# Kernel tuning notes

Measured on AMD Instinct MI355X. Metric: run time of the kernel, lower is better.

Reference implementation:

```python
import jax, jax.numpy as jnp
import numpy as np

H, DH = 8, 64  # num_heads, head_dim


def setup_inputs() -> dict:
    key = jax.random.key(0)
    ks = jax.random.split(key, 7)
    m, nq, nkv, d = 4, 2048, 2048, 512
    return {
        "xq": jax.random.normal(ks[0], (m, nq, d), jnp.float32),
        "xk": jax.random.normal(ks[1], (m, nkv, d), jnp.float32),
        "xv": jax.random.normal(ks[2], (m, nkv, d), jnp.float32),
        "Wq": jax.random.normal(ks[3], (d, H * DH), jnp.float32) * 0.02,
        "Wk": jax.random.normal(ks[4], (d, H * DH), jnp.float32) * 0.02,
        "Wv": jax.random.normal(ks[5], (d, H * DH), jnp.float32) * 0.02,
        "Wo": jax.random.normal(ks[6], (H * DH, d), jnp.float32) * 0.02,
        "bo": jnp.zeros((d,), jnp.float32),
    }


def _split_heads(t):
    # [b, n, h*d] -> [b, h, n, d]
    b, n, _ = t.shape
    return t.reshape(b, n, H, DH).transpose(0, 2, 1, 3)


def reference(xq, xk, xv, Wq, Wk, Wv, Wo, bo):
    scale = DH ** -0.5
    q = _split_heads(xq @ Wq)   # [b,h,nq,dh]
    k = _split_heads(xk @ Wk)   # [b,h,nkv,dh]
    v = _split_heads(xv @ Wv)   # [b,h,nkv,dh]
    dots = jnp.einsum("bhqd,bhkd->bhqk", q, k) * scale  # [b,h,nq,nkv]
    # diagonal attention term: query attends to its own (k,v) projection
    xq_k = _split_heads(xq @ Wk)
    xq_v = _split_heads(xq @ Wv)
    diag = jnp.sum(q * xq_k, axis=-1, keepdims=True) * scale  # [b,h,nq,1]
    dots = jnp.concatenate([dots, diag], axis=-1)  # [b,h,nq,nkv+1]
    attn = jax.nn.softmax(dots, axis=-1)
    out = jnp.einsum("bhqk,bhkd->bhqd", attn[..., :-1], v) + attn[..., -1:] * xq_v
    b, _, nq, _ = out.shape
    out = out.transpose(0, 2, 1, 3).reshape(b, nq, H * DH)  # merge heads
    return out @ Wo + bo
```

## Files before the change

### kernel.cpp

```cpp
#include <hip/hip_runtime.h>

#define LOG2E 1.44269504088896f
#define CS (0.125f * LOG2E)

typedef __bf16 bf16x8 __attribute__((ext_vector_type(8)));
typedef float f32x4 __attribute__((ext_vector_type(4)));
typedef float f32x16 __attribute__((ext_vector_type(16)));
typedef unsigned short u16x8 __attribute__((ext_vector_type(8)));

#if __has_builtin(__builtin_amdgcn_exp2f)
#define fexp2(x) __builtin_amdgcn_exp2f(x)
#else
extern "C" __device__ float __ocml_native_exp2_f32(float);
#define fexp2(x) __ocml_native_exp2_f32(x)
#endif

__device__ __forceinline__ unsigned short f2bf(float f) {
  union { float f; unsigned int u; } v{f};
  unsigned int r = v.u + 0x7fffu + ((v.u >> 16) & 1u);
  return (unsigned short)(r >> 16);
}
__device__ __forceinline__ float bf2f(unsigned short u) {
  union { unsigned int u; float f; } v; v.u = ((unsigned int)u) << 16; return v.f;
}
__device__ __forceinline__ unsigned int pkr(float a, float b) {
  unsigned int ua = __builtin_bit_cast(unsigned int, a) + 0x8000u;
  unsigned int ub = __builtin_bit_cast(unsigned int, b) + 0x8000u;
  return __builtin_amdgcn_perm(ub, ua, 0x07060302);
}

#define PLSWAP(x, y) asm("v_permlane32_swap_b32 %0, %1" : "+v"(x), "+v"(y))

typedef __attribute__((address_space(3))) unsigned int lds32_t;
typedef const __attribute__((address_space(1))) unsigned int glb32_t;
__device__ __forceinline__ void gld16(const unsigned short* g, unsigned short* l) {
  __builtin_amdgcn_global_load_lds((glb32_t*)(unsigned long long)g,
                                   (lds32_t*)(unsigned int)(unsigned long long)l,
                                   16, 0, 0);
}

__global__ __launch_bounds__(256) void conv_all(
    const float* __restrict__ xq, const float* __restrict__ xk, const float* __restrict__ xv,
    const float* __restrict__ Wq, const float* __restrict__ Wk,
    const float* __restrict__ Wv, const float* __restrict__ Wo,
    unsigned short* __restrict__ oxq, unsigned short* __restrict__ oxk, unsigned short* __restrict__ oxv,
    unsigned short* __restrict__ oWq, unsigned short* __restrict__ oWk,
    unsigned short* __restrict__ oWv, unsigned short* __restrict__ oWo) {
  __shared__ unsigned short T[64 * 65];
  const int blk = blockIdx.x;
  if (blk < 12288) {
    const int N4 = (8192 * 512) / 4;
    int idx = blk * 256 + threadIdx.x;
    const float* src; unsigned short* dst; int i;
    if (idx < N4)          { src = xq; dst = oxq; i = idx; }
    else if (idx < 2 * N4) { src = xk; dst = oxk; i = idx - N4; }
    else                   { src = xv; dst = oxv; i = idx - 2 * N4; }
    float4 v = ((const float4*)src)[i];
    ushort4 o; o.x = f2bf(v.x); o.y = f2bf(v.y); o.z = f2bf(v.z); o.w = f2bf(v.w);
    ((ushort4*)dst)[i] = o;
  } else {
    const int wblk = blk - 12288;
    const int wsel = wblk >> 6;
    const int tile = wblk & 63;
    const int tk = (tile >> 3) * 64, tn = (tile & 7) * 64;
    const float* src = (wsel == 0) ? Wq : (wsel == 1) ? Wk : (wsel == 2) ? Wv : Wo;
    unsigned short* dst = (wsel == 0) ? oWq : (wsel == 1) ? oWk : (wsel == 2) ? oWv : oWo;
    const float scale = (wsel == 0) ? CS : 1.0f;
    const int rr = threadIdx.x >> 4;
    const int cc = (threadIdx.x & 15) * 4;
#pragma unroll
    for (int i = 0; i < 4; i++) {
      int row = rr + i * 16;
      float4 v = *(const float4*)&src[(size_t)(tk + row) * 512 + tn + cc];
      T[(cc + 0) * 65 + row] = f2bf(v.x * scale);
      T[(cc + 1) * 65 + row] = f2bf(v.y * scale);
      T[(cc + 2) * 65 + row] = f2bf(v.z * scale);
      T[(cc + 3) * 65 + row] = f2bf(v.w * scale);
    }
    __syncthreads();
#pragma unroll
    for (int i = 0; i < 4; i++) {
      int n = rr + i * 16;
      ushort4 o;
      o.x = T[n * 65 + cc + 0]; o.y = T[n * 65 + cc + 1];
      o.z = T[n * 65 + cc + 2]; o.w = T[n * 65 + cc + 3];
      *(ushort4*)&dst[(size_t)(tn + n) * 512 + tk + cc] = o;
    }
  }
}

__device__ __forceinline__ void gemm_tile(
    const unsigned short* __restrict__ A, const unsigned short* __restrict__ Bt,
    int rowBlk, int colBlk, unsigned short* As, unsigned short* Bs, f32x4 (&acc)[4][4]) {
  const int t = threadIdx.x;
  const int lane = t & 63, c = lane & 15, g = lane >> 4;
  const int w = t >> 6;
  const int wm = w & 1, wn = w >> 1;
#pragma unroll
  for (int i = 0; i < 4; i++)
#pragma unroll
    for (int j = 0; j < 4; j++)
#pragma unroll
      for (int r = 0; r < 4; r++) acc[i][j][r] = 0.f;

  const int sr = t >> 2, sch = t & 3;
#define STAGE_PROJ(kkk, buf)                                                     \
  do {                                                                           \
    unsigned short* Ad = As + (buf) * (128 * 32);                                \
    unsigned short* Bd = Bs + (buf) * (128 * 32);                                \
    gld16(&A[(size_t)(rowBlk + sr) * 512 + (kkk) + sch * 8], &Ad[t * 8]);        \
    gld16(&Bt[(size_t)(colBlk + sr) * 512 + (kkk) + sch * 8], &Bd[t * 8]);       \
    gld16(&A[(size_t)(rowBlk + sr + 64) * 512 + (kkk) + sch * 8],                \
          &Ad[(t + 256) * 8]);                                                   \
    gld16(&Bt[(size_t)(colBlk + sr + 64) * 512 + (kkk) + sch * 8],               \
          &Bd[(t + 256) * 8]);                                                   \
  } while (0)

  STAGE_PROJ(0, 0);
  __syncthreads();

  for (int kt = 0; kt < 16; kt++) {
    if (kt < 15) STAGE_PROJ((kt + 1) * 32, (kt + 1) & 1);
    const unsigned short* Ac = As + (kt & 1) * (128 * 32);
    const unsigned short* Bc = Bs + (kt & 1) * (128 * 32);
    bf16x8 af[4], bfr[4];
#pragma unroll
    for (int i = 0; i < 4; i++)
      af[i] = __builtin_bit_cast(bf16x8, *(const u16x8*)&Ac[(wm * 64 + i * 16 + c) * 32 + g * 8]);
#pragma unroll
    for (int j = 0; j < 4; j++)
      bfr[j] = __builtin_bit_cast(bf16x8, *(const u16x8*)&Bc[(wn * 64 + j * 16 + c) * 32 + g * 8]);
#pragma unroll
    for (int i = 0; i < 4; i++)
#pragma unroll
      for (int j = 0; j < 4; j++)
        acc[i][j] = __builtin_amdgcn_mfma_f32_16x16x32_bf16(af[i], bfr[j], acc[i][j], 0, 0, 0);
    if (kt < 15) __syncthreads();
  }
#undef STAGE_PROJ
}

__global__ __launch_bounds__(256) void proj_all(
    const unsigned short* __restrict__ xq, const unsigned short* __restrict__ xk,
    const unsigned short* __restrict__ xv,
    const unsigned short* __restrict__ Wq, const unsigned short* __restrict__ Wk,
    const unsigned short* __restrict__ Wv,
    unsigned short* __restrict__ Qo, unsigned short* __restrict__ XKo,
    unsigned short* __restrict__ XVo, unsigned short* __restrict__ Ko,
    unsigned short* __restrict__ Vto) {
  __shared__ unsigned short As[2 * 128 * 32];
  __shared__ unsigned short Bs[2 * 128 * 32];
  const int rowBlk = blockIdx.x * 128;
  const int y = blockIdx.y;
  const unsigned short* A; const unsigned short* Bt; int colBlk; int mode;
  unsigned short* out;
  if (y < 12) {
    int wsel = y >> 2;
    A = xq; colBlk = (y & 3) * 128; mode = 0;
    Bt = (wsel == 0) ? Wq : (wsel == 1) ? Wk : Wv;
    out = (wsel == 0) ? Qo : (wsel == 1) ? XKo : XVo;
  } else if (y < 16) {
    A = xk; Bt = Wk; out = Ko; colBlk = (y - 12) * 128; mode = 0;
  } else {
    A = xv; Bt = Wv; out = Vto; colBlk = (y - 16) * 128; mode = 1;
  }
  f32x4 acc[4][4];
  gemm_tile(A, Bt, rowBlk, colBlk, As, Bs, acc);
  const int t = threadIdx.x;
  const int w = t >> 6, lane = t & 63, c = lane & 15, g = lane >> 4;
  const int wm = w & 1, wn = w >> 1;
  if (mode == 0) {
#pragma unroll
    for (int i = 0; i < 4; i++)
#pragma unroll
      for (int j = 0; j < 4; j++)
#pragma unroll
        for (int r = 0; r < 4; r++) {
          int row = rowBlk + wm * 64 + i * 16 + g * 4 + r;
          int col = colBlk + wn * 64 + j * 16 + c;
          out[(size_t)row * 512 + col] = f2bf(acc[i][j][r]);
        }
  } else {
#pragma unroll
    for (int i = 0; i < 4; i++) {
      int tok0 = rowBlk + wm * 64 + i * 16 + g * 4;
      int bb = tok0 >> 11, n0 = tok0 & 2047;
#pragma unroll
      for (int j = 0; j < 4; j++) {
        int col = colBlk + wn * 64 + j * 16 + c;
        int hh = col >> 6, dh = col & 63;
        ushort4 o;
        o.x = f2bf(acc[i][j][0]); o.y = f2bf(acc[i][j][1]);
        o.z = f2bf(acc[i][j][2]); o.w = f2bf(acc[i][j][3]);
        *(ushort4*)&out[((size_t)(bb * 8 + hh) * 64 + dh) * 2048 + n0] = o;
      }
    }
  }
}

__global__ __launch_bounds__(256) void gemm_out(
    const unsigned short* __restrict__ A, const unsigned short* __restrict__ Bt,
    float* __restrict__ out, const float* __restrict__ bias) {
  __shared__ unsigned short As[2 * 128 * 32];
  __shared__ unsigned short Bs[2 * 64 * 32];
  const int rowBlk = blockIdx.x * 128;
  const int colBlk = blockIdx.y * 64;
  const int t = threadIdx.x;
  const int lane = t & 63, c = lane & 15, g = lane >> 4;
  const int w = t >> 6;
  const int wm = w & 1, wn = w >> 1;
  f32x4 acc[4][2];
#pragma unroll
  for (int i = 0; i < 4; i++)
#pragma unroll
    for (int j = 0; j < 2; j++)
#pragma unroll
      for (int r = 0; r < 4; r++) acc[i][j][r] = 0.f;

  const int sr = t >> 2, sch = t & 3;
#define STAGE_OUT(kkk, buf)                                                      \
  do {                                                                           \
    unsigned short* Ad = As + (buf) * (128 * 32);                                \
    unsigned short* Bd = Bs + (buf) * (64 * 32);                                 \
    gld16(&A[(size_t)(rowBlk + sr) * 512 + (kkk) + sch * 8], &Ad[t * 8]);        \
    gld16(&A[(size_t)(rowBlk + sr + 64) * 512 + (kkk) + sch * 8],                \
          &Ad[(t + 256) * 8]);                                                   \
    gld16(&Bt[(size_t)(colBlk + sr) * 512 + (kkk) + sch * 8], &Bd[t * 8]);       \
  } while (0)

  STAGE_OUT(0, 0);
  __syncthreads();

  for (int kt = 0; kt < 16; kt++) {
    if (kt < 15) STAGE_OUT((kt + 1) * 32, (kt + 1) & 1);
    const unsigned short* Ac = As + (kt & 1) * (128 * 32);
    const unsigned short* Bc = Bs + (kt & 1) * (64 * 32);
    bf16x8 af[4], bfr[2];
#pragma unroll
    for (int i = 0; i < 4; i++)
      af[i] = __builtin_bit_cast(bf16x8, *(const u16x8*)&Ac[(wm * 64 + i * 16 + c) * 32 + g * 8]);
#pragma unroll
    for (int j = 0; j < 2; j++)
      bfr[j] = __builtin_bit_cast(bf16x8, *(const u16x8*)&Bc[(wn * 32 + j * 16 + c) * 32 + g * 8]);
#pragma unroll
    for (int i = 0; i < 4; i++)
#pragma unroll
      for (int j = 0; j < 2; j++)
        acc[i][j] = __builtin_amdgcn_mfma_f32_16x16x32_bf16(af[i], bfr[j], acc[i][j], 0, 0, 0);
    if (kt < 15) __syncthreads();
  }
#undef STAGE_OUT
#pragma unroll
  for (int i = 0; i < 4; i++)
#pragma unroll
    for (int j = 0; j < 2; j++)
#pragma unroll
      for (int r = 0; r < 4; r++) {
        int row = rowBlk + wm * 64 + i * 16 + g * 4 + r;
        int col = colBlk + wn * 32 + j * 16 + c;
        out[(size_t)row * 512 + col] = acc[i][j][r] + bias[col];
      }
}

__global__ __launch_bounds__(512, 2) void attn_kernel(
    const unsigned short* __restrict__ Q, const unsigned short* __restrict__ K,
    const unsigned short* __restrict__ Vt, const unsigned short* __restrict__ XK,
    const unsigned short* __restrict__ XV, unsigned short* __restrict__ O) {
  __shared__ unsigned short Ks[2][2][64 * 64];
  __shared__ unsigned short Vs[2][2][64 * 64];
  __shared__ float Fin[4][2][32];
  const int t = threadIdx.x;
  const int w = t >> 6, lane = t & 63;
  const int w01 = w & 3, wk = w >> 2;
  const int rowA = lane & 31, hi = lane >> 5, l7 = lane & 7;
  const int id = blockIdx.x;
  const int h = id & 7, qt = (id >> 3) & 15, b = id >> 7;
  const size_t hb = (size_t)b * (2048 * 512) + h * 64;
  const size_t vhb = (size_t)(b * 8 + h) * 64 * 2048;
  const int qb0 = qt * 128 + w01 * 32;

  const int sr = t >> 3, sch = t & 7;
  const int ssl = (sch ^ (sr & 7)) * 8;
  const size_t kgoff = hb + (size_t)sr * 512 + ssl;
  const size_t vgoff = vhb + (size_t)sr * 2048 + ssl;

  bf16x8 qf[4];
#pragma unroll
  for (int d = 0; d < 4; d++)
    qf[d] = __builtin_bit_cast(bf16x8,
        *(const u16x8*)&Q[hb + (size_t)(qb0 + rowA) * 512 + d * 16 + hi * 8]);

  f32x16 accO[2];
#pragma unroll
  for (int n = 0; n < 2; n++)
#pragma unroll
    for (int r = 0; r < 16; r++) accO[n][r] = 0.f;
  float lq = 0.f;

  gld16(&K[kgoff], &Ks[0][0][t * 8]);
  gld16(&K[kgoff + (size_t)16 * (64 * 512)], &Ks[1][0][t * 8]);
  gld16(&Vt[vgoff], &Vs[0][0][t * 8]);
  gld16(&Vt[vgoff + 16 * 64], &Vs[1][0][t * 8]);
  __syncthreads();

  for (int kt = 0; kt < 16; kt++) {
    const int cb = kt & 1;
    if (kt < 15) {
      gld16(&K[kgoff + (size_t)(kt + 1) * (64 * 512)], &Ks[0][cb ^ 1][t * 8]);
      gld16(&K[kgoff + (size_t)(kt + 17) * (64 * 512)], &Ks[1][cb ^ 1][t * 8]);
      gld16(&Vt[vgoff + (size_t)(kt + 1) * 64], &Vs[0][cb ^ 1][t * 8]);
      gld16(&Vt[vgoff + (size_t)(kt + 17) * 64], &Vs[1][cb ^ 1][t * 8]);
    }
    const unsigned short* Kc = &Ks[wk][cb][0];
    const unsigned short* Vc = &Vs[wk][cb][0];

    f32x16 s0, s1;
#pragma unroll
    for (int r = 0; r < 16; r++) { s0[r] = 0.f; s1[r] = 0.f; }
    __builtin_amdgcn_s_setprio(1);
#pragma unroll
    for (int d = 0; d < 4; d++) {
      bf16x8 k0 = __builtin_bit_cast(bf16x8,
          *(const u16x8*)&Kc[rowA * 64 + (((d * 2 + hi) ^ l7) * 8)]);
      s0 = __builtin_amdgcn_mfma_f32_32x32x16_bf16(k0, qf[d], s0, 0, 0, 0);
    }
#pragma unroll
    for (int d = 0; d < 4; d++) {
      bf16x8 k1 = __builtin_bit_cast(bf16x8,
          *(const u16x8*)&Kc[(32 + rowA) * 64 + (((d * 2 + hi) ^ l7) * 8)]);
      s1 = __builtin_amdgcn_mfma_f32_32x32x16_bf16(k1, qf[d], s1, 0, 0, 0);
    }
    __builtin_amdgcn_s_setprio(0);

    float sum = 0.f;
#pragma unroll
    for (int r = 0; r < 16; r++) { s0[r] = fexp2(s0[r]); sum += s0[r]; }
#pragma unroll
    for (int r = 0; r < 16; r++) { s1[r] = fexp2(s1[r]); sum += s1[r]; }
    lq += sum;

#define PVSUB(P, T2)                                                            \
  {                                                                             \
    unsigned int x0 = pkr(P[0], P[1]),   y0 = pkr(P[4], P[5]);                  \
    unsigned int x1 = pkr(P[2], P[3]),   y1 = pkr(P[6], P[7]);                  \
    unsigned int x2 = pkr(P[8], P[9]),   y2 = pkr(P[12], P[13]);                \
    unsigned int x3 = pkr(P[10], P[11]), y3 = pkr(P[14], P[15]);                \
    PLSWAP(x0, y0); PLSWAP(x1, y1); PLSWAP(x2, y2); PLSWAP(x3, y3);             \
    uint4 w0 = {x0, x1, y0, y1};                                                \
    uint4 w1 = {x2, x3, y2, y3};                                                \
    bf16x8 pa0 = __builtin_bit_cast(bf16x8, w0);                                \
    bf16x8 pa1 = __builtin_bit_cast(bf16x8, w1);                                \
    _Pragma("unroll")                                                           \
    for (int n = 0; n < 2; n++) {                                               \
      bf16x8 v0 = __builtin_bit_cast(bf16x8,                                    \
          *(const u16x8*)&Vc[(n * 32 + rowA) * 64 + ((((T2) * 4 + hi) ^ l7) * 8)]); \
      bf16x8 v1 = __builtin_bit_cast(bf16x8,                                    \
          *(const u16x8*)&Vc[(n * 32 + rowA) * 64 + ((((T2) * 4 + 2 + hi) ^ l7) * 8)]); \
      accO[n] = __builtin_amdgcn_mfma_f32_32x32x16_bf16(pa0, v0, accO[n], 0, 0, 0); \
      accO[n] = __builtin_amdgcn_mfma_f32_32x32x16_bf16(pa1, v1, accO[n], 0, 0, 0); \
    }                                                                           \
  }
    __builtin_amdgcn_s_setprio(1);
    PVSUB(s0, 0);
    PVSUB(s1, 1);
    __builtin_amdgcn_s_setprio(0);
#undef PVSUB

    if (kt < 15) __syncthreads();
  }

  __syncthreads();

  {
    float* MB = (w01 < 2) ? (float*)&Ks[0][0][0] : (float*)&Vs[0][0][0];
    const int mbase = ((w01 & 1) * 64 + lane) * 33;
    if (wk == 1) {
#pragma unroll
      for (int n = 0; n < 2; n++)
#pragma unroll
        for (int reg = 0; reg < 16; reg++) MB[mbase + n * 16 + reg] = accO[n][reg];
      MB[mbase + 32] = lq;
    }
    __syncthreads();
    if (wk == 1) return;
#pragma unroll
    for (int n = 0; n < 2; n++)
#pragma unroll
      for (int reg = 0; reg < 16; reg++) accO[n][reg] += MB[mbase + n * 16 + reg];
    lq += MB[mbase + 32];
  }

  lq += __shfl_xor(lq, 32);

  float part = 0.f;
  {
    const size_t base = hb + (size_t)(qb0 + rowA) * 512 + hi * 32;
#pragma unroll
    for (int ii = 0; ii < 4; ii++) {
      u16x8 q8 = *(const u16x8*)&Q[base + ii * 8];
      u16x8 x8 = *(const u16x8*)&XK[base + ii * 8];
#pragma unroll
      for (int e = 0; e < 8; e++) part += bf2f(q8[e]) * bf2f(x8[e]);
    }
  }
  part += __shfl_xor(part, 32);
  float pd = fexp2(part);
  float inv = 1.f / (lq + pd);
  if (lane < 32) {
    Fin[w01][0][rowA] = inv;
    Fin[w01][1][rowA] = pd * inv;
  }
  __builtin_amdgcn_s_waitcnt(0);

  f32x4 inva[4], pia[4];
#pragma unroll
  for (int rq = 0; rq < 4; rq++) {
    inva[rq] = *(const f32x4*)&Fin[w01][0][rq * 8 + hi * 4];
    pia[rq]  = *(const f32x4*)&Fin[w01][1][rq * 8 + hi * 4];
  }
#pragma unroll
  for (int n = 0; n < 2; n++)
#pragma unroll
    for (int reg = 0; reg < 16; reg++) {
      const int rq = reg >> 2, r = reg & 3;
      const int q = rq * 8 + hi * 4 + r;
      const int qrow = qb0 + q;
      float xv = bf2f(XV[hb + (size_t)qrow * 512 + n * 32 + rowA]);
      float val = accO[n][reg] * inva[rq][r] + pia[rq][r] * xv;
      O[((size_t)(b * 2048 + qrow)) * 512 + h * 64 + n * 32 + rowA] = f2bf(val);
    }
}

extern "C" void kernel_launch(void* const* d_in, const int* in_sizes, int n_in,
                              void* d_out, int out_size, void* d_ws, size_t ws_size,
                              hipStream_t stream) {
  const float* xq = (const float*)d_in[0];
  const float* xk = (const float*)d_in[1];
  const float* xv = (const float*)d_in[2];
  const float* Wq = (const float*)d_in[3];
  const float* Wk = (const float*)d_in[4];
  const float* Wv = (const float*)d_in[5];
  const float* Wo = (const float*)d_in[6];
  const float* bo = (const float*)d_in[7];

  unsigned short* ws = (unsigned short*)d_ws;
  const size_t MD = 8192ull * 512;
  const size_t WD = 512ull * 512;
  unsigned short* xq_b = ws;
  unsigned short* xk_b = xq_b + MD;
  unsigned short* xv_b = xk_b + MD;
  unsigned short* Wq_t = xv_b + MD;
  unsigned short* Wk_t = Wq_t + WD;
  unsigned short* Wv_t = Wk_t + WD;
  unsigned short* Wo_t = Wv_t + WD;
  unsigned short* Qb  = Wo_t + WD;
  unsigned short* Kb  = Qb + MD;
  unsigned short* Vtb = Kb + MD;
  unsigned short* XKb = Vtb + MD;
  unsigned short* XVb = XKb + MD;
  unsigned short* Ob  = XVb + MD;

  conv_all<<<dim3(12544), 256, 0, stream>>>(xq, xk, xv, Wq, Wk, Wv, Wo,
                                            xq_b, xk_b, xv_b, Wq_t, Wk_t, Wv_t, Wo_t);
  proj_all<<<dim3(64, 20), 256, 0, stream>>>(xq_b, xk_b, xv_b, Wq_t, Wk_t, Wv_t,
                                             Qb, XKb, XVb, Kb, Vtb);
  attn_kernel<<<dim3(512), 512, 0, stream>>>(Qb, Kb, Vtb, XKb, XVb, Ob);
  gemm_out<<<dim3(64, 8), 256, 0, stream>>>(Ob, Wo_t, (float*)d_out, bo);
}
```

Before: 202.0 us.

## Fuse fp32-to-bf16 activation conversion into projection GEMM operand loading

Removes the separate pass that converted the xq/xk/xv activations to bf16. The projection GEMM now loads fp32 activations into registers, converts them and stores them to LDS with register double-buffering. The weight-only conversion kernel remains, and the Q scale moves from the weight conversion to the projection output. This cuts a full read/write round trip over the activations, but each projection block re-reads fp32 data (twice the bytes) and loses the direct global-to-LDS path for the A operand.

Result: faster. 191.9 us (-5.0%).

```diff
diff --git a/kernel.cpp b/kernel.cpp
--- a/kernel.cpp
+++ b/kernel.cpp
@@ -39,136 +39,137 @@
                                    16, 0, 0);
 }
 
-__global__ __launch_bounds__(256) void conv_all(
-    const float* __restrict__ xq, const float* __restrict__ xk, const float* __restrict__ xv,
+__global__ __launch_bounds__(256) void conv_w(
     const float* __restrict__ Wq, const float* __restrict__ Wk,
     const float* __restrict__ Wv, const float* __restrict__ Wo,
-    unsigned short* __restrict__ oxq, unsigned short* __restrict__ oxk, unsigned short* __restrict__ oxv,
     unsigned short* __restrict__ oWq, unsigned short* __restrict__ oWk,
     unsigned short* __restrict__ oWv, unsigned short* __restrict__ oWo) {
   __shared__ unsigned short T[64 * 65];
-  const int blk = blockIdx.x;
-  if (blk < 12288) {
-    const int N4 = (8192 * 512) / 4;
-    int idx = blk * 256 + threadIdx.x;
-    const float* src; unsigned short* dst; int i;
-    if (idx < N4)          { src = xq; dst = oxq; i = idx; }
-    else if (idx < 2 * N4) { src = xk; dst = oxk; i = idx - N4; }
-    else                   { src = xv; dst = oxv; i = idx - 2 * N4; }
-    float4 v = ((const float4*)src)[i];
-    ushort4 o; o.x = f2bf(v.x); o.y = f2bf(v.y); o.z = f2bf(v.z); o.w = f2bf(v.w);
-    ((ushort4*)dst)[i] = o;
-  } else {
-    const int wblk = blk - 12288;
-    const int wsel = wblk >> 6;
-    const int tile = wblk & 63;
-    const int tk = (tile >> 3) * 64, tn = (tile & 7) * 64;
-    const float* src = (wsel == 0) ? Wq : (wsel == 1) ? Wk : (wsel == 2) ? Wv : Wo;
-    unsigned short* dst = (wsel == 0) ? oWq : (wsel == 1) ? oWk : (wsel == 2) ? oWv : oWo;
-    const float scale = (wsel == 0) ? CS : 1.0f;
-    const int rr = threadIdx.x >> 4;
-    const int cc = (threadIdx.x & 15) * 4;
-#pragma unroll
-    for (int i = 0; i < 4; i++) {
-      int row = rr + i * 16;
-      float4 v = *(const float4*)&src[(size_t)(tk + row) * 512 + tn + cc];
-      T[(cc + 0) * 65 + row] = f2bf(v.x * scale);
-      T[(cc + 1) * 65 + row] = f2bf(v.y * scale);
-      T[(cc + 2) * 65 + row] = f2bf(v.z * scale);
-      T[(cc + 3) * 65 + row] = f2bf(v.w * scale);
-    }
-    __syncthreads();
-#pragma unroll
-    for (int i = 0; i < 4; i++) {
-      int n = rr + i * 16;
-      ushort4 o;
-      o.x = T[n * 65 + cc + 0]; o.y = T[n * 65 + cc + 1];
-      o.z = T[n * 65 + cc + 2]; o.w = T[n * 65 + cc + 3];
-      *(ushort4*)&dst[(size_t)(tn + n) * 512 + tk + cc] = o;
-    }
-  }
-}
-
-__device__ __forceinline__ void gemm_tile(
-    const unsigned short* __restrict__ A, const unsigned short* __restrict__ Bt,
-    int rowBlk, int colBlk, unsigned short* As, unsigned short* Bs, f32x4 (&acc)[4][4]) {
-  const int t = threadIdx.x;
-  const int lane = t & 63, c = lane & 15, g = lane >> 4;
-  const int w = t >> 6;
-  const int wm = w & 1, wn = w >> 1;
-#pragma unroll
-  for (int i = 0; i < 4; i++)
-#pragma unroll
-    for (int j = 0; j < 4; j++)
-#pragma unroll
-      for (int r = 0; r < 4; r++) acc[i][j][r] = 0.f;
-
-  const int sr = t >> 2, sch = t & 3;
-#define STAGE_PROJ(kkk, buf)                                                     \
-  do {                                                                           \
-    unsigned short* Ad = As + (buf) * (128 * 32);                                \
-    unsigned short* Bd = Bs + (buf) * (128 * 32);                                \
-    gld16(&A[(size_t)(rowBlk + sr) * 512 + (kkk) + sch * 8], &Ad[t * 8]);        \
-    gld16(&Bt[(size_t)(colBlk + sr) * 512 + (kkk) + sch * 8], &Bd[t * 8]);       \
-    gld16(&A[(size_t)(rowBlk + sr + 64) * 512 + (kkk) + sch * 8],                \
-          &Ad[(t + 256) * 8]);                                                   \
-    gld16(&Bt[(size_t)(colBlk + sr + 64) * 512 + (kkk) + sch * 8],               \
-          &Bd[(t + 256) * 8]);                                                   \
-  } while (0)
-
-  STAGE_PROJ(0, 0);
+  const int wblk = blockIdx.x;
+  const int wsel = wblk >> 6;
+  const int tile = wblk & 63;
+  const int tk = (tile >> 3) * 64, tn = (tile & 7) * 64;
+  const float* src = (wsel == 0) ? Wq : (wsel == 1) ? Wk : (wsel == 2) ? Wv : Wo;
+  unsigned short* dst = (wsel == 0) ? oWq : (wsel == 1) ? oWk : (wsel == 2) ? oWv : oWo;
+  const int rr = threadIdx.x >> 4;
+  const int cc = (threadIdx.x & 15) * 4;
+#pragma unroll
+  for (int i = 0; i < 4; i++) {
+    int row = rr + i * 16;
+    float4 v = *(const float4*)&src[(size_t)(tk + row) * 512 + tn + cc];
+    T[(cc + 0) * 65 + row] = f2bf(v.x);
+    T[(cc + 1) * 65 + row] = f2bf(v.y);
+    T[(cc + 2) * 65 + row] = f2bf(v.z);
+    T[(cc + 3) * 65 + row] = f2bf(v.w);
+  }
   __syncthreads();
-
-  for (int kt = 0; kt < 16; kt++) {
-    if (kt < 15) STAGE_PROJ((kt + 1) * 32, (kt + 1) & 1);
-    const unsigned short* Ac = As + (kt & 1) * (128 * 32);
-    const unsigned short* Bc = Bs + (kt & 1) * (128 * 32);
-    bf16x8 af[4], bfr[4];
-#pragma unroll
-    for (int i = 0; i < 4; i++)
-      af[i] = __builtin_bit_cast(bf16x8, *(const u16x8*)&Ac[(wm * 64 + i * 16 + c) * 32 + g * 8]);
-#pragma unroll
-    for (int j = 0; j < 4; j++)
-      bfr[j] = __builtin_bit_cast(bf16x8, *(const u16x8*)&Bc[(wn * 64 + j * 16 + c) * 32 + g * 8]);
-#pragma unroll
-    for (int i = 0; i < 4; i++)
-#pragma unroll
-      for (int j = 0; j < 4; j++)
-        acc[i][j] = __builtin_amdgcn_mfma_f32_16x16x32_bf16(af[i], bfr[j], acc[i][j], 0, 0, 0);
-    if (kt < 15) __syncthreads();
-  }
-#undef STAGE_PROJ
+#pragma unroll
+  for (int i = 0; i < 4; i++) {
+    int n = rr + i * 16;
+    ushort4 o;
+    o.x = T[n * 65 + cc + 0]; o.y = T[n * 65 + cc + 1];
+    o.z = T[n * 65 + cc + 2]; o.w = T[n * 65 + cc + 3];
+    *(ushort4*)&dst[(size_t)(tn + n) * 512 + tk + cc] = o;
+  }
 }
 
 __global__ __launch_bounds__(256) void proj_all(
-    const unsigned short* __restrict__ xq, const unsigned short* __restrict__ xk,
-    const unsigned short* __restrict__ xv,
+    const float* __restrict__ xqf, const float* __restrict__ xkf,
+    const float* __restrict__ xvf,
     const unsigned short* __restrict__ Wq, const unsigned short* __restrict__ Wk,
     const unsigned short* __restrict__ Wv,
     unsigned short* __restrict__ Qo, unsigned short* __restrict__ XKo,
     unsigned short* __restrict__ XVo, unsigned short* __restrict__ Ko,
     unsigned short* __restrict__ Vto) {
-  __shared__ unsigned short As[2 * 128 * 32];
-  __shared__ unsigned short Bs[2 * 128 * 32];
+  __shared__ unsigned short As[2][128 * 32];
+  __shared__ unsigned short Bs[2][128 * 32];
   const int rowBlk = blockIdx.x * 128;
   const int y = blockIdx.y;
-  const unsigned short* A; const unsigned short* Bt; int colBlk; int mode;
+  const float* Af; const unsigned short* Bt; int colBlk; int mode;
+  float osc = 1.0f;
   unsigned short* out;
   if (y < 12) {
     int wsel = y >> 2;
-    A = xq; colBlk = (y & 3) * 128; mode = 0;
+    Af = xqf; colBlk = (y & 3) * 128; mode = 0;
     Bt = (wsel == 0) ? Wq : (wsel == 1) ? Wk : Wv;
     out = (wsel == 0) ? Qo : (wsel == 1) ? XKo : XVo;
+    if (wsel == 0) osc = CS;
   } else if (y < 16) {
-    A = xk; Bt = Wk; out = Ko; colBlk = (y - 12) * 128; mode = 0;
+    Af = xkf; Bt = Wk; out = Ko; colBlk = (y - 12) * 128; mode = 0;
   } else {
-    A = xv; Bt = Wv; out = Vto; colBlk = (y - 16) * 128; mode = 1;
-  }
+    Af = xvf; Bt = Wv; out = Vto; colBlk = (y - 16) * 128; mode = 1;
+  }
+  const int t = threadIdx.x;
+  const int lane = t & 63, c = lane & 15, g = lane >> 4;
+  const int w = t >> 6;
+  const int wm = w & 1, wn = w >> 1;
   f32x4 acc[4][4];
-  gemm_tile(A, Bt, rowBlk, colBlk, As, Bs, acc);
-  const int t = threadIdx.x;
-  const int w = t >> 6, lane = t & 63, c = lane & 15, g = lane >> 4;
-  const int wm = w & 1, wn = w >> 1;
+#pragma unroll
+  for (int i = 0; i < 4; i++)
+#pragma unroll
+    for (int j = 0; j < 4; j++)
+#pragma unroll
+      for (int r = 0; r < 4; r++) acc[i][j][r] = 0.f;
+
+  const int sr = t >> 2, sch = t & 3;
+  const float* pa0 = &Af[(size_t)(rowBlk + sr) * 512 + sch * 8];
+  const float* pa1 = &Af[(size_t)(rowBlk + sr + 64) * 512 + sch * 8];
+
+#define LOAD_A(kkk)                                                              \
+    va0 = *(const float4*)&pa0[(kkk)];     va1 = *(const float4*)&pa0[(kkk) + 4];\
+    va2 = *(const float4*)&pa1[(kkk)];     va3 = *(const float4*)&pa1[(kkk) + 4];
+#define STORE_A(buf)                                                             \
+  {                                                                              \
+    u16x8 u0, u1;                                                                \
+    u0[0] = f2bf(va0.x); u0[1] = f2bf(va0.y); u0[2] = f2bf(va0.z);               \
+    u0[3] = f2bf(va0.w); u0[4] = f2bf(va1.x); u0[5] = f2bf(va1.y);               \
+    u0[6] = f2bf(va1.z); u0[7] = f2bf(va1.w);                                    \
+    u1[0] = f2bf(va2.x); u1[1] = f2bf(va2.y); u1[2] = f2bf(va2.z);               \
+    u1[3] = f2bf(va2.w); u1[4] = f2bf(va3.x); u1[5] = f2bf(va3.y);               \
+    u1[6] = f2bf(va3.z); u1[7] = f2bf(va3.w);                                    \
+    *(u16x8*)&As[buf][t * 8] = u0;                                               \
+    *(u16x8*)&As[buf][(t + 256) * 8] = u1;                                       \
+  }
+#define STAGE_B(kkk, buf)                                                        \
+  do {                                                                           \
+    gld16(&Bt[(size_t)(colBlk + sr) * 512 + (kkk) + sch * 8], &Bs[buf][t * 8]);  \
+    gld16(&Bt[(size_t)(colBlk + sr + 64) * 512 + (kkk) + sch * 8],               \
+          &Bs[buf][(t + 256) * 8]);                                              \
+  } while (0)
+
+  float4 va0, va1, va2, va3;
+  LOAD_A(0);
+  STAGE_B(0, 0);
+  STORE_A(0);
+  __syncthreads();
+
+  for (int kt = 0; kt < 16; kt++) {
+    const int cb = kt & 1;
+    if (kt < 15) {
+      LOAD_A((kt + 1) * 32);
+      STAGE_B((kt + 1) * 32, cb ^ 1);
+    }
+    bf16x8 af[4], bfr[4];
+#pragma unroll
+    for (int i = 0; i < 4; i++)
+      af[i] = __builtin_bit_cast(bf16x8, *(const u16x8*)&As[cb][(wm * 64 + i * 16 + c) * 32 + g * 8]);
+#pragma unroll
+    for (int j = 0; j < 4; j++)
+      bfr[j] = __builtin_bit_cast(bf16x8, *(const u16x8*)&Bs[cb][(wn * 64 + j * 16 + c) * 32 + g * 8]);
+#pragma unroll
+    for (int i = 0; i < 4; i++)
+#pragma unroll
+      for (int j = 0; j < 4; j++)
+        acc[i][j] = __builtin_amdgcn_mfma_f32_16x16x32_bf16(af[i], bfr[j], acc[i][j], 0, 0, 0);
+    if (kt < 15) {
+      STORE_A(cb ^ 1);
+      __syncthreads();
+    }
+  }
+#undef LOAD_A
+#undef STORE_A
+#undef STAGE_B
+
   if (mode == 0) {
 #pragma unroll
     for (int i = 0; i < 4; i++)
@@ -178,7 +179,7 @@
         for (int r = 0; r < 4; r++) {
           int row = rowBlk + wm * 64 + i * 16 + g * 4 + r;
           int col = colBlk + wn * 64 + j * 16 + c;
-          out[(size_t)row * 512 + col] = f2bf(acc[i][j][r]);
+          out[(size_t)row * 512 + col] = f2bf(acc[i][j][r] * osc);
         }
   } else {
 #pragma unroll
@@ -446,10 +447,7 @@
   unsigned short* ws = (unsigned short*)d_ws;
   const size_t MD = 8192ull * 512;
   const size_t WD = 512ull * 512;
-  unsigned short* xq_b = ws;
-  unsigned short* xk_b = xq_b + MD;
-  unsigned short* xv_b = xk_b + MD;
-  unsigned short* Wq_t = xv_b + MD;
+  unsigned short* Wq_t = ws;
   unsigned short* Wk_t = Wq_t + WD;
   unsigned short* Wv_t = Wk_t + WD;
   unsigned short* Wo_t = Wv_t + WD;
@@ -460,9 +458,8 @@
   unsigned short* XVb = XKb + MD;
   unsigned short* Ob  = XVb + MD;
 
-  conv_all<<<dim3(12544), 256, 0, stream>>>(xq, xk, xv, Wq, Wk, Wv, Wo,
-                                            xq_b, xk_b, xv_b, Wq_t, Wk_t, Wv_t, Wo_t);
-  proj_all<<<dim3(64, 20), 256, 0, stream>>>(xq_b, xk_b, xv_b, Wq_t, Wk_t, Wv_t,
+  conv_w<<<dim3(256), 256, 0, stream>>>(Wq, Wk, Wv, Wo, Wq_t, Wk_t, Wv_t, Wo_t);
+  proj_all<<<dim3(64, 20), 256, 0, stream>>>(xq, xk, xv, Wq_t, Wk_t, Wv_t,
                                              Qb, XKb, XVb, Kb, Vtb);
   attn_kernel<<<dim3(512), 512, 0, stream>>>(Qb, Kb, Vtb, XKb, XVb, Ob);
   gemm_out<<<dim3(64, 8), 256, 0, stream>>>(Ob, Wo_t, (float*)d_out, bo);
```
